# Performance work log

Measured on AMD Instinct MI355X. Metric: run time of the kernel, lower is better.

The kernel has to match this reference:

```python
import jax, jax.numpy as jnp
import numpy as np

EPS = 0.001
NEG_SLOPE = 0.01

def _conv2d(x, w):
    # x: [B, Cin, H, W], w: [Cout, Cin, kh, kw], SAME padding, stride 1
    return jax.lax.conv_general_dilated(
        x, w, window_strides=(1, 1), padding='SAME',
        dimension_numbers=('NCHW', 'OIHW', 'NCHW'))

def setup_inputs() -> dict:
    key = jax.random.key(0)
    k1, k2, k3 = jax.random.split(key, 3)
    B, T, C, H, W = 8, 16, 32, 64, 64
    HID, K = 64, 3
    x = jax.random.normal(k1, (B, T, C, H, W), dtype=jnp.float32)
    fan_in = (C + HID) * K * K
    w_conv = jax.random.normal(k2, (4 * HID, C + HID, K, K), dtype=jnp.float32) / np.sqrt(fan_in)
    b_conv = jax.random.normal(k3, (4 * HID,), dtype=jnp.float32) * 0.01
    gamma = jnp.ones((HID,), dtype=jnp.float32)
    beta = jnp.zeros((HID,), dtype=jnp.float32)
    return {'x': x, 'w_conv': w_conv, 'b_conv': b_conv, 'gamma': gamma, 'beta': beta}

def reference(x, w_conv, b_conv, gamma, beta):
    B, T, C, H, W = x.shape
    HID = w_conv.shape[0] // 4

    def step(carry, xt):
        h, c = carry
        combined = jnp.concatenate([xt, h], axis=1)            # [B, C+HID, H, W]
        cc = _conv2d(combined, w_conv) + b_conv[None, :, None, None]
        cc_i, cc_f, cc_o, cc_g = jnp.split(cc, 4, axis=1)
        c_new = jax.nn.sigmoid(cc_f) * c + jax.nn.sigmoid(cc_i) * jnp.tanh(cc_g)
        h_new = jax.nn.sigmoid(cc_o) * jnp.tanh(c_new)
        out = jnp.where(h_new >= 0, h_new, NEG_SLOPE * h_new)  # LeakyReLU(0.01)
        return (h_new, c_new), out

    h0 = jnp.zeros((B, HID, H, W), dtype=x.dtype)
    c0 = jnp.zeros_like(h0)
    xs = jnp.transpose(x, (1, 0, 2, 3, 4))                     # [T, B, C, H, W]
    _, outs = jax.lax.scan(step, (h0, c0), xs)                 # [T, B, HID, H, W]
    out = jnp.transpose(outs, (1, 0, 2, 3, 4))                 # [B, T, HID, H, W]

    # BatchNorm3d in training mode: stats over (B, T, H, W) per channel (biased var)
    mean = jnp.mean(out, axis=(0, 1, 3, 4), keepdims=True)
    var = jnp.mean(jnp.square(out - mean), axis=(0, 1, 3, 4), keepdims=True)
    g = gamma[None, None, :, None, None]
    bta = beta[None, None, :, None, None]
    out = (out - mean) * jax.lax.rsqrt(var + EPS) * g + bta
    return out
```

## Files before the change

kernel.cpp:

```cpp
#include <hip/hip_runtime.h>

#define BB 8
#define TT 16
#define CIN 32
#define HID 64
#define HH 64
#define WW 64
#define EPS 1e-3f
#define NEG_SLOPE 0.01f

typedef short s16x8 __attribute__((ext_vector_type(8)));
typedef _Float16 hx8 __attribute__((ext_vector_type(8)));
typedef float fx4 __attribute__((ext_vector_type(4)));

__device__ __forceinline__ float tanh_fast(float x) {
    x = fminf(fmaxf(x, -15.f), 15.f);
    float e = __expf(-2.f * x);
    return (1.f - e) / (1.f + e);
}

__global__ __launch_bounds__(256) void x2h(const float* __restrict__ x,
                                           _Float16* __restrict__ xcl) {
    __shared__ float s[32][65];
    int y = blockIdx.x, t = blockIdx.y, b = blockIdx.z;
    int tid = threadIdx.x;
    const float* src = x + (((size_t)(b * TT + t) * CIN) * HH + y) * WW;
#pragma unroll
    for (int k = 0; k < 8; ++k) {
        int idx = tid + k * 256;
        int c = idx >> 6, xx = idx & 63;
        s[c][xx] = src[(size_t)c * HH * WW + xx];
    }
    __syncthreads();
    int xx = tid >> 2, c0 = (tid & 3) * 8;
    _Float16 tmp[8];
#pragma unroll
    for (int j = 0; j < 8; ++j) tmp[j] = (_Float16)s[c0 + j][xx];
    _Float16* dst = xcl + (((size_t)(b * TT + t) * 4096) + y * 64 + xx) * 32 + c0;
    *(hx8*)dst = *(hx8*)tmp;
}

__global__ __launch_bounds__(256) void pack_wh(const float* __restrict__ w,
                                               _Float16* __restrict__ wpk) {
    int idx = blockIdx.x * 256 + threadIdx.x;
    if (idx >= 256 * 864) return;
    int k7 = idx & 7;
    int j = idx >> 3;
    int n = j & 255;
    int kk = j >> 8;
    int tap = kk / 12;
    int r12 = kk % 12;
    int ks = (r12 >> 2) * 32 + (r12 & 3) * 8 + k7;
    int gate = (n >> 4) & 3;
    int hid  = (n >> 6) * 16 + (n & 15);
    int oc   = gate * 64 + hid;
    wpk[idx] = (_Float16)w[((size_t)oc * 96 + ks) * 9 + tap];
}

__global__ __launch_bounds__(512, 4) void lstm_step(
    const _Float16* __restrict__ xcl,
    const _Float16* __restrict__ wpk,
    const float* __restrict__ bias,
    const _Float16* __restrict__ h_in,
    _Float16* __restrict__ h_out,
    float* __restrict__ c_ws,
    float* __restrict__ out,
    float* __restrict__ partial,
    int t) {
    const int y0 = blockIdx.x, b = blockIdx.y;
    const int tid = threadIdx.x;
    const int lane15 = tid & 15;
    const int kq = (tid >> 4) & 3;
    const int w = tid >> 6;
    const int w4 = w & 3;
    const int mh = w >> 2;

    __shared__ __align__(16) unsigned short s_t[3 * 66 * 104];

    const short* xb_t = (const short*)xcl + (size_t)(b * TT + t) * 4096 * 32;
    for (int u = tid; u < 3 * 66 * 4; u += 512) {
        int unit = u & 3, pix = u >> 2;
        int col = pix % 66, r = pix / 66;
        int iy = y0 + r - 1, ix = col - 1;
        s16x8 v = (s16x8)0;
        if (iy >= 0 && iy < 64 && ix >= 0 && ix < 64)
            v = *(const s16x8*)(xb_t + ((size_t)iy * 64 + ix) * 32 + unit * 8);
        *(s16x8*)(s_t + (r * 66 + col) * 104 + unit * 8) = v;
    }
    if (t > 0) {
        for (int u = tid; u < 3 * 66 * 8; u += 512) {
            int unit = u & 7, pix = u >> 3;
            int col = pix % 66, r = pix / 66;
            int iy = y0 + r - 1, ix = col - 1;
            s16x8 v = (s16x8)0;
            if (iy >= 0 && iy < 64 && ix >= 0 && ix < 64)
                v = *(const s16x8*)((const short*)h_in +
                                    ((size_t)(b * 64 + iy) * 64 + ix) * 64 + unit * 8);
            *(s16x8*)(s_t + (r * 66 + col) * 104 + 32 + unit * 8) = v;
        }
    }
    __syncthreads();

    fx4 acc[2][4];
#pragma unroll
    for (int m = 0; m < 2; ++m)
#pragma unroll
        for (int g = 0; g < 4; ++g) acc[m][g] = (fx4)0.f;

    const int nbase = 4 * w4 * 16 + lane15;
    const int colb0 = (mh * 2 + 0) * 16 + lane15;
    const int colb1 = (mh * 2 + 1) * 16 + lane15;

    if (t > 0) {
#pragma unroll 1
        for (int tap = 0; tap < 9; ++tap) {
            const int ky = tap / 3, kx = tap % 3;
            const unsigned short* a0 = s_t + (ky * 66 + colb0 + kx) * 104 + kq * 8;
            const unsigned short* a1 = s_t + (ky * 66 + colb1 + kx) * 104 + kq * 8;
            const _Float16* wp = wpk + ((size_t)(tap * 12 + kq) * 256 + nbase) * 8;
#pragma unroll
            for (int kc = 0; kc < 3; ++kc) {
                hx8 bf[4];
#pragma unroll
                for (int g = 0; g < 4; ++g)
                    bf[g] = *(const hx8*)(wp + (size_t)(kc * 4) * 256 * 8 + g * 16 * 8);
                hx8 af0 = *(const hx8*)(a0 + kc * 32);
                hx8 af1 = *(const hx8*)(a1 + kc * 32);
#pragma unroll
                for (int g = 0; g < 4; ++g) {
                    acc[0][g] = __builtin_amdgcn_mfma_f32_16x16x32_f16(af0, bf[g], acc[0][g], 0, 0, 0);
                    acc[1][g] = __builtin_amdgcn_mfma_f32_16x16x32_f16(af1, bf[g], acc[1][g], 0, 0, 0);
                }
            }
        }
    } else {
#pragma unroll 1
        for (int tap = 0; tap < 9; ++tap) {
            const int ky = tap / 3, kx = tap % 3;
            const unsigned short* a0 = s_t + (ky * 66 + colb0 + kx) * 104 + kq * 8;
            const unsigned short* a1 = s_t + (ky * 66 + colb1 + kx) * 104 + kq * 8;
            const _Float16* wp = wpk + ((size_t)(tap * 12 + kq) * 256 + nbase) * 8;
            hx8 bf[4];
#pragma unroll
            for (int g = 0; g < 4; ++g)
                bf[g] = *(const hx8*)(wp + g * 16 * 8);
            hx8 af0 = *(const hx8*)a0;
            hx8 af1 = *(const hx8*)a1;
#pragma unroll
            for (int g = 0; g < 4; ++g) {
                acc[0][g] = __builtin_amdgcn_mfma_f32_16x16x32_f16(af0, bf[g], acc[0][g], 0, 0, 0);
                acc[1][g] = __builtin_amdgcn_mfma_f32_16x16x32_f16(af1, bf[g], acc[1][g], 0, 0, 0);
            }
        }
    }

    const int hid = w4 * 16 + lane15;
    const float bi = bias[hid], bff = bias[64 + hid];
    const float bo = bias[128 + hid], bg = bias[192 + hid];
    float osum = 0.f, osum2 = 0.f;
#pragma unroll
    for (int m = 0; m < 2; ++m) {
        int xb = (mh * 2 + m) * 16 + kq * 4;
        size_t pixbase = (size_t)(b * 64 + y0) * 64 + xb;
        float4 o4;
#pragma unroll
        for (int r = 0; r < 4; ++r) {
            float ci = acc[m][0][r] + bi;
            float cf = acc[m][1][r] + bff;
            float co = acc[m][2][r] + bo;
            float cg_ = acc[m][3][r] + bg;
            size_t ca = (pixbase + r) * 64 + hid;
            float c_old = (t > 0) ? c_ws[ca] : 0.f;
            float si = 1.f / (1.f + __expf(-ci));
            float sf = 1.f / (1.f + __expf(-cf));
            float so = 1.f / (1.f + __expf(-co));
            float c_new = sf * c_old + si * tanh_fast(cg_);
            float h = so * tanh_fast(c_new);
            if (t < TT - 1) {
                c_ws[ca] = c_new;
                h_out[ca] = (_Float16)h;
            }
            float ov = (h >= 0.f) ? h : NEG_SLOPE * h;
            (&o4.x)[r] = ov;
            osum += ov;
            osum2 += ov * ov;
        }
        *(float4*)(out + (((size_t)(b * TT + t) * 64 + hid) * 64 + y0) * 64 + xb) = o4;
    }
    osum  += __shfl_xor(osum, 16);  osum  += __shfl_xor(osum, 32);
    osum2 += __shfl_xor(osum2, 16); osum2 += __shfl_xor(osum2, 32);
    if (kq == 0) {
        int row2 = (b * 64 + y0) * 2 + mh;
        if (t == 0) {
            partial[row2 * 128 + hid] = osum;
            partial[row2 * 128 + 64 + hid] = osum2;
        } else {
            partial[row2 * 128 + hid] += osum;
            partial[row2 * 128 + 64 + hid] += osum2;
        }
    }
}

__global__ __launch_bounds__(512) void finalize_stats(const float* __restrict__ partial,
                                                      float* __restrict__ stats,
                                                      const float* __restrict__ gamma,
                                                      const float* __restrict__ beta) {
    int idx = threadIdx.x & 127;
    int seg = threadIdx.x >> 7;
    float s = 0.f;
    for (int k = seg * 256; k < seg * 256 + 256; ++k) s += partial[k * 128 + idx];
    __shared__ float red[4][128];
    red[seg][idx] = s;
    __syncthreads();
    if (threadIdx.x < 64) {
        int hid = threadIdx.x;
        const float n = (float)((size_t)BB * TT * HH * WW);
        float mean = (red[0][hid] + red[1][hid] + red[2][hid] + red[3][hid]) / n;
        float var  = (red[0][64 + hid] + red[1][64 + hid] + red[2][64 + hid] + red[3][64 + hid]) / n
                     - mean * mean;
        float inv  = rsqrtf(var + EPS);
        float sc   = gamma[hid] * inv;
        stats[hid]      = sc;
        stats[64 + hid] = beta[hid] - mean * sc;
    }
}

__global__ __launch_bounds__(256) void normalize_k(float* __restrict__ out,
                                                   const float* __restrict__ stats) {
    const size_t N = (size_t)BB * TT * HID * HH * WW;
    size_t i = ((size_t)blockIdx.x * blockDim.x + threadIdx.x) * 4;
    size_t stride = (size_t)gridDim.x * blockDim.x * 4;
    for (; i < N; i += stride) {
        int ch = (int)((i >> 12) & (HID - 1));
        float sc = stats[ch], sh = stats[64 + ch];
        float4 v = *(float4*)(out + i);
        v.x = fmaf(v.x, sc, sh);
        v.y = fmaf(v.y, sc, sh);
        v.z = fmaf(v.z, sc, sh);
        v.w = fmaf(v.w, sc, sh);
        *(float4*)(out + i) = v;
    }
}

extern "C" void kernel_launch(void* const* d_in, const int* in_sizes, int n_in,
                              void* d_out, int out_size, void* d_ws, size_t ws_size,
                              hipStream_t stream) {
    const float* x     = (const float*)d_in[0];
    const float* w     = (const float*)d_in[1];
    const float* bias  = (const float*)d_in[2];
    const float* gamma = (const float*)d_in[3];
    const float* beta  = (const float*)d_in[4];
    float* out = (float*)d_out;
    char* wsb = (char*)d_ws;

    _Float16* xcl   = (_Float16*)(wsb);
    _Float16* wpk   = (_Float16*)(wsb + 33554432);
    _Float16* hA    = (_Float16*)(wsb + 33996800);
    _Float16* hB    = (_Float16*)(wsb + 38191104);
    float* c_ws     = (float*)(wsb + 42385408);
    float* partial  = (float*)(wsb + 50774016);
    float* stats    = (float*)(wsb + 51298304);

    x2h<<<dim3(64, 16, 8), 256, 0, stream>>>(x, xcl);
    pack_wh<<<864, 256, 0, stream>>>(w, wpk);

    _Float16* hin = hA;
    _Float16* hout = hB;
    for (int t = 0; t < TT; ++t) {
        lstm_step<<<dim3(64, 8), 512, 0, stream>>>(xcl, wpk, bias, hin, hout,
                                                   c_ws, out, partial, t);
        _Float16* tmp = hin; hin = hout; hout = tmp;
    }
    finalize_stats<<<1, 512, 0, stream>>>(partial, stats, gamma, beta);
    normalize_k<<<8192, 256, 0, stream>>>(out, stats);
}
```

Before: 650.8 us.

## Fuse two LSTM timesteps per launch using halo recomputation in LDS

Each block now computes two consecutive timesteps for two output rows. It recomputes a one-row halo of the first step so the second step's hidden state can be read from LDS instead of global memory. This halves the number of step launches and the global h/c round-trips, and it ping-pongs the c buffer to avoid read-after-write hazards. The cost is roughly 1.5x redundant MFMA work in the first step, more LDS (about 137KB dynamic), more accumulator registers, and only 256 blocks per launch.

```diff
diff --git a/kernel.cpp b/kernel.cpp
--- a/kernel.cpp
+++ b/kernel.cpp
@@ -57,66 +57,81 @@
     wpk[idx] = (_Float16)w[((size_t)oc * 96 + ks) * 9 + tap];
 }
 
-__global__ __launch_bounds__(512, 4) void lstm_step(
+__global__ __launch_bounds__(512, 2) void lstm_pair(
     const _Float16* __restrict__ xcl,
     const _Float16* __restrict__ wpk,
     const float* __restrict__ bias,
     const _Float16* __restrict__ h_in,
     _Float16* __restrict__ h_out,
-    float* __restrict__ c_ws,
+    const float* __restrict__ c_in,
+    float* __restrict__ c_out,
     float* __restrict__ out,
     float* __restrict__ partial,
-    int t) {
-    const int y0 = blockIdx.x, b = blockIdx.y;
+    int t0) {
+    extern __shared__ __align__(16) unsigned short lds[];
+    unsigned short* tA = lds;
+    unsigned short* tB = lds + 6 * 66 * 104;
+
+    const int rb = blockIdx.x, b = blockIdx.y;
+    const int base = rb * 2;
     const int tid = threadIdx.x;
     const int lane15 = tid & 15;
     const int kq = (tid >> 4) & 3;
     const int w = tid >> 6;
     const int w4 = w & 3;
-    const int mh = w >> 2;
-
-    __shared__ __align__(16) unsigned short s_t[3 * 66 * 104];
-
-    const short* xb_t = (const short*)xcl + (size_t)(b * TT + t) * 4096 * 32;
-    for (int u = tid; u < 3 * 66 * 4; u += 512) {
-        int unit = u & 3, pix = u >> 2;
-        int col = pix % 66, r = pix / 66;
-        int iy = y0 + r - 1, ix = col - 1;
+    const int u = w >> 2;
+
+    const short* xb_t = (const short*)xcl + (size_t)(b * TT + t0) * 4096 * 32;
+    for (int i = tid; i < 6 * 66 * 4; i += 512) {
+        int unit = i & 3, pix = i >> 2;
+        int col = pix % 66, ra = pix / 66;
+        int iy = base - 2 + ra, ix = col - 1;
         s16x8 v = (s16x8)0;
         if (iy >= 0 && iy < 64 && ix >= 0 && ix < 64)
             v = *(const s16x8*)(xb_t + ((size_t)iy * 64 + ix) * 32 + unit * 8);
-        *(s16x8*)(s_t + (r * 66 + col) * 104 + unit * 8) = v;
-    }
-    if (t > 0) {
-        for (int u = tid; u < 3 * 66 * 8; u += 512) {
-            int unit = u & 7, pix = u >> 3;
-            int col = pix % 66, r = pix / 66;
-            int iy = y0 + r - 1, ix = col - 1;
+        *(s16x8*)(tA + (ra * 66 + col) * 104 + unit * 8) = v;
+    }
+    if (t0 > 0) {
+        for (int i = tid; i < 6 * 66 * 8; i += 512) {
+            int unit = i & 7, pix = i >> 3;
+            int col = pix % 66, ra = pix / 66;
+            int iy = base - 2 + ra, ix = col - 1;
             s16x8 v = (s16x8)0;
             if (iy >= 0 && iy < 64 && ix >= 0 && ix < 64)
                 v = *(const s16x8*)((const short*)h_in +
                                     ((size_t)(b * 64 + iy) * 64 + ix) * 64 + unit * 8);
-            *(s16x8*)(s_t + (r * 66 + col) * 104 + 32 + unit * 8) = v;
-        }
+            *(s16x8*)(tA + (ra * 66 + col) * 104 + 32 + unit * 8) = v;
+        }
+    }
+    const short* xb_t1 = (const short*)xcl + (size_t)(b * TT + t0 + 1) * 4096 * 32;
+    for (int i = tid; i < 4 * 66 * 4; i += 512) {
+        int unit = i & 3, pix = i >> 2;
+        int col = pix % 66, rw = pix / 66;
+        int iy = base - 1 + rw, ix = col - 1;
+        s16x8 v = (s16x8)0;
+        if (iy >= 0 && iy < 64 && ix >= 0 && ix < 64)
+            v = *(const s16x8*)(xb_t1 + ((size_t)iy * 64 + ix) * 32 + unit * 8);
+        *(s16x8*)(tB + (rw * 66 + col) * 104 + unit * 8) = v;
+    }
+    for (int i = tid; i < 4 * 66 * 8; i += 512) {
+        int unit = i & 7, pix = i >> 3;
+        int col = pix % 66, rw = pix / 66;
+        *(s16x8*)(tB + (rw * 66 + col) * 104 + 32 + unit * 8) = (s16x8)0;
     }
     __syncthreads();
 
-    fx4 acc[2][4];
-#pragma unroll
-    for (int m = 0; m < 2; ++m)
-#pragma unroll
-        for (int g = 0; g < 4; ++g) acc[m][g] = (fx4)0.f;
+    fx4 acc[8][4];
+#pragma unroll
+    for (int j = 0; j < 8; ++j)
+#pragma unroll
+        for (int g = 0; g < 4; ++g) acc[j][g] = (fx4)0.f;
 
     const int nbase = 4 * w4 * 16 + lane15;
-    const int colb0 = (mh * 2 + 0) * 16 + lane15;
-    const int colb1 = (mh * 2 + 1) * 16 + lane15;
-
-    if (t > 0) {
+
+    if (t0 > 0) {
 #pragma unroll 1
         for (int tap = 0; tap < 9; ++tap) {
             const int ky = tap / 3, kx = tap % 3;
-            const unsigned short* a0 = s_t + (ky * 66 + colb0 + kx) * 104 + kq * 8;
-            const unsigned short* a1 = s_t + (ky * 66 + colb1 + kx) * 104 + kq * 8;
             const _Float16* wp = wpk + ((size_t)(tap * 12 + kq) * 256 + nbase) * 8;
 #pragma unroll
             for (int kc = 0; kc < 3; ++kc) {
@@ -124,12 +139,14 @@
 #pragma unroll
                 for (int g = 0; g < 4; ++g)
                     bf[g] = *(const hx8*)(wp + (size_t)(kc * 4) * 256 * 8 + g * 16 * 8);
-                hx8 af0 = *(const hx8*)(a0 + kc * 32);
-                hx8 af1 = *(const hx8*)(a1 + kc * 32);
-#pragma unroll
-                for (int g = 0; g < 4; ++g) {
-                    acc[0][g] = __builtin_amdgcn_mfma_f32_16x16x32_f16(af0, bf[g], acc[0][g], 0, 0, 0);
-                    acc[1][g] = __builtin_amdgcn_mfma_f32_16x16x32_f16(af1, bf[g], acc[1][g], 0, 0, 0);
+#pragma unroll
+                for (int j = 0; j < 8; ++j) {
+                    int ra = 2 * u + (j >> 2) + ky;
+                    int ccol = (j & 3) * 16 + lane15 + kx;
+                    hx8 af = *(const hx8*)(tA + (ra * 66 + ccol) * 104 + kc * 32 + kq * 8);
+#pragma unroll
+                    for (int g = 0; g < 4; ++g)
+                        acc[j][g] = __builtin_amdgcn_mfma_f32_16x16x32_f16(af, bf[g], acc[j][g], 0, 0, 0);
                 }
             }
         }
@@ -137,19 +154,19 @@
 #pragma unroll 1
         for (int tap = 0; tap < 9; ++tap) {
             const int ky = tap / 3, kx = tap % 3;
-            const unsigned short* a0 = s_t + (ky * 66 + colb0 + kx) * 104 + kq * 8;
-            const unsigned short* a1 = s_t + (ky * 66 + colb1 + kx) * 104 + kq * 8;
             const _Float16* wp = wpk + ((size_t)(tap * 12 + kq) * 256 + nbase) * 8;
             hx8 bf[4];
 #pragma unroll
             for (int g = 0; g < 4; ++g)
                 bf[g] = *(const hx8*)(wp + g * 16 * 8);
-            hx8 af0 = *(const hx8*)a0;
-            hx8 af1 = *(const hx8*)a1;
-#pragma unroll
-            for (int g = 0; g < 4; ++g) {
-                acc[0][g] = __builtin_amdgcn_mfma_f32_16x16x32_f16(af0, bf[g], acc[0][g], 0, 0, 0);
-                acc[1][g] = __builtin_amdgcn_mfma_f32_16x16x32_f16(af1, bf[g], acc[1][g], 0, 0, 0);
+#pragma unroll
+            for (int j = 0; j < 8; ++j) {
+                int ra = 2 * u + (j >> 2) + ky;
+                int ccol = (j & 3) * 16 + lane15 + kx;
+                hx8 af = *(const hx8*)(tA + (ra * 66 + ccol) * 104 + kq * 8);
+#pragma unroll
+                for (int g = 0; g < 4; ++g)
+                    acc[j][g] = __builtin_amdgcn_mfma_f32_16x16x32_f16(af, bf[g], acc[j][g], 0, 0, 0);
             }
         }
     }
@@ -157,46 +174,114 @@
     const int hid = w4 * 16 + lane15;
     const float bi = bias[hid], bff = bias[64 + hid];
     const float bo = bias[128 + hid], bg = bias[192 + hid];
+    fx4 creg[4];
     float osum = 0.f, osum2 = 0.f;
 #pragma unroll
-    for (int m = 0; m < 2; ++m) {
-        int xb = (mh * 2 + m) * 16 + kq * 4;
-        size_t pixbase = (size_t)(b * 64 + y0) * 64 + xb;
+    for (int j = 0; j < 8; ++j) {
+        int trow = 2 * u + (j >> 2), colq = j & 3;
+        int oy = base - 1 + trow;
+        bool exist = (oy >= 0 && oy < 64);
+        bool interior = ((j >> 2) == 1 - u);
+        int col = colq * 16 + kq * 4;
         float4 o4;
 #pragma unroll
-        for (int r = 0; r < 4; ++r) {
-            float ci = acc[m][0][r] + bi;
-            float cf = acc[m][1][r] + bff;
-            float co = acc[m][2][r] + bo;
-            float cg_ = acc[m][3][r] + bg;
-            size_t ca = (pixbase + r) * 64 + hid;
-            float c_old = (t > 0) ? c_ws[ca] : 0.f;
+        for (int r4 = 0; r4 < 4; ++r4) {
+            float ci = acc[j][0][r4] + bi;
+            float cf = acc[j][1][r4] + bff;
+            float co = acc[j][2][r4] + bo;
+            float cg_ = acc[j][3][r4] + bg;
+            size_t ca = ((size_t)(b * 64 + oy) * 64 + col + r4) * 64 + hid;
+            float c_old = (t0 > 0 && exist) ? c_in[ca] : 0.f;
             float si = 1.f / (1.f + __expf(-ci));
             float sf = 1.f / (1.f + __expf(-cf));
             float so = 1.f / (1.f + __expf(-co));
             float c_new = sf * c_old + si * tanh_fast(cg_);
             float h = so * tanh_fast(c_new);
-            if (t < TT - 1) {
-                c_ws[ca] = c_new;
-                h_out[ca] = (_Float16)h;
-            }
-            float ov = (h >= 0.f) ? h : NEG_SLOPE * h;
-            (&o4.x)[r] = ov;
-            osum += ov;
-            osum2 += ov * ov;
-        }
-        *(float4*)(out + (((size_t)(b * TT + t) * 64 + hid) * 64 + y0) * 64 + xb) = o4;
-    }
+            if (exist)
+                ((_Float16*)tB)[(trow * 66 + col + r4 + 1) * 104 + 32 + hid] = (_Float16)h;
+            if (interior) {
+                creg[colq][r4] = c_new;
+                float ov = (h >= 0.f) ? h : NEG_SLOPE * h;
+                (&o4.x)[r4] = ov;
+                osum += ov;
+                osum2 += ov * ov;
+            }
+        }
+        if (interior)
+            *(float4*)(out + (((size_t)(b * TT + t0) * 64 + hid) * 64 + oy) * 64 + col) = o4;
+    }
+    __syncthreads();
+
+    fx4 acc2[4][4];
+#pragma unroll
+    for (int j = 0; j < 4; ++j)
+#pragma unroll
+        for (int g = 0; g < 4; ++g) acc2[j][g] = (fx4)0.f;
+
+#pragma unroll 1
+    for (int tap = 0; tap < 9; ++tap) {
+        const int ky = tap / 3, kx = tap % 3;
+        const _Float16* wp = wpk + ((size_t)(tap * 12 + kq) * 256 + nbase) * 8;
+#pragma unroll
+        for (int kc = 0; kc < 3; ++kc) {
+            hx8 bf[4];
+#pragma unroll
+            for (int g = 0; g < 4; ++g)
+                bf[g] = *(const hx8*)(wp + (size_t)(kc * 4) * 256 * 8 + g * 16 * 8);
+            int ra = u + ky;
+#pragma unroll
+            for (int j = 0; j < 4; ++j) {
+                int ccol = j * 16 + lane15 + kx;
+                hx8 af = *(const hx8*)(tB + (ra * 66 + ccol) * 104 + kc * 32 + kq * 8);
+#pragma unroll
+                for (int g = 0; g < 4; ++g)
+                    acc2[j][g] = __builtin_amdgcn_mfma_f32_16x16x32_f16(af, bf[g], acc2[j][g], 0, 0, 0);
+            }
+        }
+    }
+
+    {
+        int oy = base + u;
+#pragma unroll
+        for (int j = 0; j < 4; ++j) {
+            int col = j * 16 + kq * 4;
+            float4 o4;
+#pragma unroll
+            for (int r4 = 0; r4 < 4; ++r4) {
+                float ci = acc2[j][0][r4] + bi;
+                float cf = acc2[j][1][r4] + bff;
+                float co = acc2[j][2][r4] + bo;
+                float cg_ = acc2[j][3][r4] + bg;
+                float c_old = creg[j][r4];
+                float si = 1.f / (1.f + __expf(-ci));
+                float sf = 1.f / (1.f + __expf(-cf));
+                float so = 1.f / (1.f + __expf(-co));
+                float c_new = sf * c_old + si * tanh_fast(cg_);
+                float h = so * tanh_fast(c_new);
+                size_t ca = ((size_t)(b * 64 + oy) * 64 + col + r4) * 64 + hid;
+                if (t0 + 1 < TT - 1) {
+                    c_out[ca] = c_new;
+                    h_out[ca] = (_Float16)h;
+                }
+                float ov = (h >= 0.f) ? h : NEG_SLOPE * h;
+                (&o4.x)[r4] = ov;
+                osum += ov;
+                osum2 += ov * ov;
+            }
+            *(float4*)(out + (((size_t)(b * TT + t0 + 1) * 64 + hid) * 64 + oy) * 64 + col) = o4;
+        }
+    }
+
     osum  += __shfl_xor(osum, 16);  osum  += __shfl_xor(osum, 32);
     osum2 += __shfl_xor(osum2, 16); osum2 += __shfl_xor(osum2, 32);
     if (kq == 0) {
-        int row2 = (b * 64 + y0) * 2 + mh;
-        if (t == 0) {
-            partial[row2 * 128 + hid] = osum;
-            partial[row2 * 128 + 64 + hid] = osum2;
+        int slot = b * 64 + base + u;
+        if (t0 == 0) {
+            partial[slot * 128 + hid] = osum;
+            partial[slot * 128 + 64 + hid] = osum2;
         } else {
-            partial[row2 * 128 + hid] += osum;
-            partial[row2 * 128 + 64 + hid] += osum2;
+            partial[slot * 128 + hid] += osum;
+            partial[slot * 128 + 64 + hid] += osum2;
         }
     }
 }
@@ -208,7 +293,7 @@
     int idx = threadIdx.x & 127;
     int seg = threadIdx.x >> 7;
     float s = 0.f;
-    for (int k = seg * 256; k < seg * 256 + 256; ++k) s += partial[k * 128 + idx];
+    for (int k = seg * 128; k < seg * 128 + 128; ++k) s += partial[k * 128 + idx];
     __shared__ float red[4][128];
     red[seg][idx] = s;
     __syncthreads();
@@ -257,19 +342,30 @@
     _Float16* wpk   = (_Float16*)(wsb + 33554432);
     _Float16* hA    = (_Float16*)(wsb + 33996800);
     _Float16* hB    = (_Float16*)(wsb + 38191104);
-    float* c_ws     = (float*)(wsb + 42385408);
-    float* partial  = (float*)(wsb + 50774016);
-    float* stats    = (float*)(wsb + 51298304);
+    float* cA       = (float*)(wsb + 42385408);
+    float* cB       = (float*)(wsb + 50774016);
+    float* partial  = (float*)(wsb + 59162624);
+    float* stats    = (float*)(wsb + 59424768);
+
+    const int LDSZ = (6 * 66 * 104 + 4 * 66 * 104) * 2;
 
     x2h<<<dim3(64, 16, 8), 256, 0, stream>>>(x, xcl);
     pack_wh<<<864, 256, 0, stream>>>(w, wpk);
 
-    _Float16* hin = hA;
-    _Float16* hout = hB;
-    for (int t = 0; t < TT; ++t) {
-        lstm_step<<<dim3(64, 8), 512, 0, stream>>>(xcl, wpk, bias, hin, hout,
-                                                   c_ws, out, partial, t);
-        _Float16* tmp = hin; hin = hout; hout = tmp;
+    static bool attr_set = false;
+    if (!attr_set) {
+        hipFuncSetAttribute(reinterpret_cast<const void*>(lstm_pair),
+                            hipFuncAttributeMaxDynamicSharedMemorySize, LDSZ);
+        attr_set = true;
+    }
+
+    _Float16* hin = hA;  _Float16* hout = hB;
+    float* cin = cA;     float* cout = cB;
+    for (int p = 0; p < 8; ++p) {
+        lstm_pair<<<dim3(32, 8), 512, LDSZ, stream>>>(xcl, wpk, bias, hin, hout,
+                                                      cin, cout, out, partial, 2 * p);
+        _Float16* th = hin; hin = hout; hout = th;
+        float* tc = cin; cin = cout; cout = tc;
     }
     finalize_stats<<<1, 512, 0, stream>>>(partial, stats, gamma, beta);
     normalize_k<<<8192, 256, 0, stream>>>(out, stats);
```

New measurement: 687.8 us. +5.7%, slower.

## Fuse all LSTM timesteps into one persistent kernel with neighbor flag sync

Applied to the files above, without the earlier changes.

Replaces the 16 per-timestep launches with one persistent kernel of 256 blocks. Each block owns two image rows, keeps the cell state in registers and its own h in shared memory, and only exchanges boundary rows through a global halo buffer guarded by per-row flags. This removes launch overhead and the global round-trips of c and h each step. The cost is that progress now depends on all 256 blocks being resident at once, since blocks spin-wait on their neighbours' flags, plus relaxed-atomic halo traffic.

```diff
diff --git a/kernel.cpp b/kernel.cpp
--- a/kernel.cpp
+++ b/kernel.cpp
@@ -12,6 +12,7 @@
 typedef short s16x8 __attribute__((ext_vector_type(8)));
 typedef _Float16 hx8 __attribute__((ext_vector_type(8)));
 typedef float fx4 __attribute__((ext_vector_type(4)));
+typedef unsigned long long u64;
 
 __device__ __forceinline__ float tanh_fast(float x) {
     x = fminf(fmaxf(x, -15.f), 15.f);
@@ -57,147 +58,165 @@
     wpk[idx] = (_Float16)w[((size_t)oc * 96 + ks) * 9 + tap];
 }
 
-__global__ __launch_bounds__(512, 4) void lstm_step(
+__global__ __launch_bounds__(512, 2) void lstm_all(
     const _Float16* __restrict__ xcl,
     const _Float16* __restrict__ wpk,
     const float* __restrict__ bias,
-    const _Float16* __restrict__ h_in,
-    _Float16* __restrict__ h_out,
-    float* __restrict__ c_ws,
+    u64* __restrict__ haloA,
+    u64* __restrict__ haloB,
     float* __restrict__ out,
     float* __restrict__ partial,
-    int t) {
-    const int y0 = blockIdx.x, b = blockIdx.y;
+    int* __restrict__ flags) {
+    const int r = blockIdx.x, b = blockIdx.y;
     const int tid = threadIdx.x;
     const int lane15 = tid & 15;
     const int kq = (tid >> 4) & 3;
     const int w = tid >> 6;
     const int w4 = w & 3;
-    const int mh = w >> 2;
-
-    __shared__ __align__(16) unsigned short s_t[3 * 66 * 104];
-
-    const short* xb_t = (const short*)xcl + (size_t)(b * TT + t) * 4096 * 32;
-    for (int u = tid; u < 3 * 66 * 4; u += 512) {
-        int unit = u & 3, pix = u >> 2;
-        int col = pix % 66, r = pix / 66;
-        int iy = y0 + r - 1, ix = col - 1;
-        s16x8 v = (s16x8)0;
-        if (iy >= 0 && iy < 64 && ix >= 0 && ix < 64)
-            v = *(const s16x8*)(xb_t + ((size_t)iy * 64 + ix) * 32 + unit * 8);
-        *(s16x8*)(s_t + (r * 66 + col) * 104 + unit * 8) = v;
-    }
-    if (t > 0) {
-        for (int u = tid; u < 3 * 66 * 8; u += 512) {
-            int unit = u & 7, pix = u >> 3;
-            int col = pix % 66, r = pix / 66;
-            int iy = y0 + r - 1, ix = col - 1;
+    const int u = w >> 2;
+    const int yy = 2 * r + u;
+
+    __shared__ __align__(16) unsigned short s_t[4 * 66 * 104];
+
+    const int hid = w4 * 16 + lane15;
+    const float bi = bias[hid], bff = bias[64 + hid];
+    const float bo = bias[128 + hid], bg = bias[192 + hid];
+    const int nbase = 4 * w4 * 16 + lane15;
+
+    fx4 creg[4];
+#pragma unroll
+    for (int j = 0; j < 4; ++j) creg[j] = (fx4)0.f;
+    float osum = 0.f, osum2 = 0.f;
+
+    for (int i = tid; i < 4 * 66 * 8; i += 512) {
+        int unit = i & 7, pix = i >> 3;
+        *(s16x8*)(s_t + pix * 104 + 32 + unit * 8) = (s16x8)0;
+    }
+
+#pragma unroll 1
+    for (int t = 0; t < TT; ++t) {
+        if (t > 0) {
+            if (tid < 2) {
+                int nb = r + (tid ? 1 : -1);
+                if (nb >= 0 && nb < 32) {
+                    const int fid = b * 32 + nb;
+                    int spins = 0;
+                    while (__hip_atomic_load(&flags[fid], __ATOMIC_RELAXED,
+                                             __HIP_MEMORY_SCOPE_AGENT) < t) {
+                        __builtin_amdgcn_s_sleep(2);
+                        if (++spins > (1 << 20)) break;
+                    }
+                }
+            }
+            __syncthreads();
+        }
+
+        const short* xb_t = (const short*)xcl + (size_t)(b * TT + t) * 4096 * 32;
+        for (int i = tid; i < 4 * 66 * 4; i += 512) {
+            int unit = i & 3, pix = i >> 2;
+            int col = pix % 66, ra = pix / 66;
+            int iy = 2 * r - 1 + ra, ix = col - 1;
             s16x8 v = (s16x8)0;
             if (iy >= 0 && iy < 64 && ix >= 0 && ix < 64)
-                v = *(const s16x8*)((const short*)h_in +
-                                    ((size_t)(b * 64 + iy) * 64 + ix) * 64 + unit * 8);
-            *(s16x8*)(s_t + (r * 66 + col) * 104 + 32 + unit * 8) = v;
-        }
-    }
-    __syncthreads();
-
-    fx4 acc[2][4];
-#pragma unroll
-    for (int m = 0; m < 2; ++m)
-#pragma unroll
-        for (int g = 0; g < 4; ++g) acc[m][g] = (fx4)0.f;
-
-    const int nbase = 4 * w4 * 16 + lane15;
-    const int colb0 = (mh * 2 + 0) * 16 + lane15;
-    const int colb1 = (mh * 2 + 1) * 16 + lane15;
-
-    if (t > 0) {
+                v = *(const s16x8*)(xb_t + ((size_t)iy * 64 + ix) * 32 + unit * 8);
+            *(s16x8*)(s_t + pix * 104 + unit * 8) = v;
+        }
+        if (t > 0) {
+            const u64* hb = ((t - 1) & 1) ? haloB : haloA;
+            for (int i = tid; i < 2 * 64 * 16; i += 512) {
+                int pg = i & 15, ch = (i >> 4) & 63, side = i >> 10;
+                int ra = side ? 3 : 0;
+                int iy = side ? (2 * r + 2) : (2 * r - 1);
+                u64 v = 0;
+                if (iy >= 0 && iy < 64)
+                    v = __hip_atomic_load(&hb[((size_t)(b * 64 + iy) * 64 + ch) * 16 + pg],
+                                          __ATOMIC_RELAXED, __HIP_MEMORY_SCOPE_AGENT);
+                union { u64 q; unsigned short s[4]; } uv; uv.q = v;
+                int colb = 1 + pg * 4;
+#pragma unroll
+                for (int k = 0; k < 4; ++k)
+                    s_t[(ra * 66 + colb + k) * 104 + 32 + ch] = uv.s[k];
+            }
+        }
+        __syncthreads();
+
+        fx4 acc[4][4];
+#pragma unroll
+        for (int j = 0; j < 4; ++j)
+#pragma unroll
+            for (int g = 0; g < 4; ++g) acc[j][g] = (fx4)0.f;
+
 #pragma unroll 1
         for (int tap = 0; tap < 9; ++tap) {
             const int ky = tap / 3, kx = tap % 3;
-            const unsigned short* a0 = s_t + (ky * 66 + colb0 + kx) * 104 + kq * 8;
-            const unsigned short* a1 = s_t + (ky * 66 + colb1 + kx) * 104 + kq * 8;
             const _Float16* wp = wpk + ((size_t)(tap * 12 + kq) * 256 + nbase) * 8;
+            const unsigned short* abase = s_t + ((u + ky) * 66 + lane15 + kx) * 104 + kq * 8;
 #pragma unroll
             for (int kc = 0; kc < 3; ++kc) {
                 hx8 bf[4];
 #pragma unroll
                 for (int g = 0; g < 4; ++g)
                     bf[g] = *(const hx8*)(wp + (size_t)(kc * 4) * 256 * 8 + g * 16 * 8);
-                hx8 af0 = *(const hx8*)(a0 + kc * 32);
-                hx8 af1 = *(const hx8*)(a1 + kc * 32);
-#pragma unroll
-                for (int g = 0; g < 4; ++g) {
-                    acc[0][g] = __builtin_amdgcn_mfma_f32_16x16x32_f16(af0, bf[g], acc[0][g], 0, 0, 0);
-                    acc[1][g] = __builtin_amdgcn_mfma_f32_16x16x32_f16(af1, bf[g], acc[1][g], 0, 0, 0);
+#pragma unroll
+                for (int j = 0; j < 4; ++j) {
+                    hx8 af = *(const hx8*)(abase + j * 16 * 104 + kc * 32);
+#pragma unroll
+                    for (int g = 0; g < 4; ++g)
+                        acc[j][g] = __builtin_amdgcn_mfma_f32_16x16x32_f16(af, bf[g], acc[j][g], 0, 0, 0);
                 }
             }
         }
-    } else {
-#pragma unroll 1
-        for (int tap = 0; tap < 9; ++tap) {
-            const int ky = tap / 3, kx = tap % 3;
-            const unsigned short* a0 = s_t + (ky * 66 + colb0 + kx) * 104 + kq * 8;
-            const unsigned short* a1 = s_t + (ky * 66 + colb1 + kx) * 104 + kq * 8;
-            const _Float16* wp = wpk + ((size_t)(tap * 12 + kq) * 256 + nbase) * 8;
-            hx8 bf[4];
-#pragma unroll
-            for (int g = 0; g < 4; ++g)
-                bf[g] = *(const hx8*)(wp + g * 16 * 8);
-            hx8 af0 = *(const hx8*)a0;
-            hx8 af1 = *(const hx8*)a1;
-#pragma unroll
-            for (int g = 0; g < 4; ++g) {
-                acc[0][g] = __builtin_amdgcn_mfma_f32_16x16x32_f16(af0, bf[g], acc[0][g], 0, 0, 0);
-                acc[1][g] = __builtin_amdgcn_mfma_f32_16x16x32_f16(af1, bf[g], acc[1][g], 0, 0, 0);
-            }
-        }
-    }
-
-    const int hid = w4 * 16 + lane15;
-    const float bi = bias[hid], bff = bias[64 + hid];
-    const float bo = bias[128 + hid], bg = bias[192 + hid];
-    float osum = 0.f, osum2 = 0.f;
-#pragma unroll
-    for (int m = 0; m < 2; ++m) {
-        int xb = (mh * 2 + m) * 16 + kq * 4;
-        size_t pixbase = (size_t)(b * 64 + y0) * 64 + xb;
-        float4 o4;
-#pragma unroll
-        for (int r = 0; r < 4; ++r) {
-            float ci = acc[m][0][r] + bi;
-            float cf = acc[m][1][r] + bff;
-            float co = acc[m][2][r] + bo;
-            float cg_ = acc[m][3][r] + bg;
-            size_t ca = (pixbase + r) * 64 + hid;
-            float c_old = (t > 0) ? c_ws[ca] : 0.f;
-            float si = 1.f / (1.f + __expf(-ci));
-            float sf = 1.f / (1.f + __expf(-cf));
-            float so = 1.f / (1.f + __expf(-co));
-            float c_new = sf * c_old + si * tanh_fast(cg_);
-            float h = so * tanh_fast(c_new);
-            if (t < TT - 1) {
-                c_ws[ca] = c_new;
-                h_out[ca] = (_Float16)h;
-            }
-            float ov = (h >= 0.f) ? h : NEG_SLOPE * h;
-            (&o4.x)[r] = ov;
-            osum += ov;
-            osum2 += ov * ov;
-        }
-        *(float4*)(out + (((size_t)(b * TT + t) * 64 + hid) * 64 + y0) * 64 + xb) = o4;
-    }
+        __syncthreads();
+
+        u64* hbc = (t & 1) ? haloB : haloA;
+#pragma unroll
+        for (int j = 0; j < 4; ++j) {
+            int px0 = j * 16 + kq * 4;
+            float4 o4;
+            union { u64 q; unsigned short s[4]; } hp;
+#pragma unroll
+            for (int r4 = 0; r4 < 4; ++r4) {
+                float ci = acc[j][0][r4] + bi;
+                float cf = acc[j][1][r4] + bff;
+                float co = acc[j][2][r4] + bo;
+                float cg_ = acc[j][3][r4] + bg;
+                float c_old = creg[j][r4];
+                float si = 1.f / (1.f + __expf(-ci));
+                float sf = 1.f / (1.f + __expf(-cf));
+                float so = 1.f / (1.f + __expf(-co));
+                float c_new = sf * c_old + si * tanh_fast(cg_);
+                float h = so * tanh_fast(c_new);
+                creg[j][r4] = c_new;
+                _Float16 hh = (_Float16)h;
+                union { _Float16 f; unsigned short s; } hc; hc.f = hh;
+                hp.s[r4] = hc.s;
+                if (t < TT - 1)
+                    s_t[((1 + u) * 66 + 1 + px0 + r4) * 104 + 32 + hid] = hc.s;
+                float ov = (h >= 0.f) ? h : NEG_SLOPE * h;
+                (&o4.x)[r4] = ov;
+                osum += ov;
+                osum2 += ov * ov;
+            }
+            if (t < TT - 1)
+                __hip_atomic_store(&hbc[((size_t)(b * 64 + yy) * 64 + hid) * 16 + (j * 4 + kq)],
+                                   hp.q, __ATOMIC_RELAXED, __HIP_MEMORY_SCOPE_AGENT);
+            *(float4*)(out + (((size_t)(b * TT + t) * 64 + hid) * 64 + yy) * 64 + px0) = o4;
+        }
+
+        if (t < TT - 1) {
+            __syncthreads();
+            if (tid == 0)
+                __hip_atomic_store(&flags[b * 32 + r], t + 1,
+                                   __ATOMIC_RELAXED, __HIP_MEMORY_SCOPE_AGENT);
+        }
+    }
+
     osum  += __shfl_xor(osum, 16);  osum  += __shfl_xor(osum, 32);
     osum2 += __shfl_xor(osum2, 16); osum2 += __shfl_xor(osum2, 32);
     if (kq == 0) {
-        int row2 = (b * 64 + y0) * 2 + mh;
-        if (t == 0) {
-            partial[row2 * 128 + hid] = osum;
-            partial[row2 * 128 + 64 + hid] = osum2;
-        } else {
-            partial[row2 * 128 + hid] += osum;
-            partial[row2 * 128 + 64 + hid] += osum2;
-        }
+        int slot = b * 64 + yy;
+        partial[slot * 128 + hid] = osum;
+        partial[slot * 128 + 64 + hid] = osum2;
     }
 }
 
@@ -208,7 +227,7 @@
     int idx = threadIdx.x & 127;
     int seg = threadIdx.x >> 7;
     float s = 0.f;
-    for (int k = seg * 256; k < seg * 256 + 256; ++k) s += partial[k * 128 + idx];
+    for (int k = seg * 128; k < seg * 128 + 128; ++k) s += partial[k * 128 + idx];
     __shared__ float red[4][128];
     red[seg][idx] = s;
     __syncthreads();
@@ -253,24 +272,22 @@
     float* out = (float*)d_out;
     char* wsb = (char*)d_ws;
 
-    _Float16* xcl   = (_Float16*)(wsb);
-    _Float16* wpk   = (_Float16*)(wsb + 33554432);
-    _Float16* hA    = (_Float16*)(wsb + 33996800);
-    _Float16* hB    = (_Float16*)(wsb + 38191104);
-    float* c_ws     = (float*)(wsb + 42385408);
-    float* partial  = (float*)(wsb + 50774016);
-    float* stats    = (float*)(wsb + 51298304);
+    _Float16* xcl  = (_Float16*)(wsb);
+    _Float16* wpk  = (_Float16*)(wsb + 33554432);
+    u64* haloA     = (u64*)(wsb + 33996800);
+    u64* haloB     = (u64*)(wsb + 38191104);
+    float* partial = (float*)(wsb + 42385408);
+    float* stats   = (float*)(wsb + 42647552);
+    int*   flags   = (int*)(wsb + 42648064);
+
+    hipMemsetAsync(flags, 0, 1024, stream);
 
     x2h<<<dim3(64, 16, 8), 256, 0, stream>>>(x, xcl);
     pack_wh<<<864, 256, 0, stream>>>(w, wpk);
 
-    _Float16* hin = hA;
-    _Float16* hout = hB;
-    for (int t = 0; t < TT; ++t) {
-        lstm_step<<<dim3(64, 8), 512, 0, stream>>>(xcl, wpk, bias, hin, hout,
-                                                   c_ws, out, partial, t);
-        _Float16* tmp = hin; hin = hout; hout = tmp;
-    }
+    lstm_all<<<dim3(32, 8), 512, 0, stream>>>(xcl, wpk, bias, haloA, haloB,
+                                              out, partial, flags);
+
     finalize_stats<<<1, 512, 0, stream>>>(partial, stats, gamma, beta);
     normalize_k<<<8192, 256, 0, stream>>>(out, stats);
 }
```

After: 581.8 us. 10.6% less time.
